# Kernel optimization log

Measured on AMD Instinct MI355X. Metric: run time of the kernel, lower is better.

The kernel has to match this reference:

```python
import jax, jax.numpy as jnp
import numpy as np

HIDDEN = 1024
N_HEADS = 16
HEAD = HIDDEN // N_HEADS  # 64
DFF = 4 * HIDDEN


def setup_inputs() -> dict:
    key = jax.random.key(0)
    ks = jax.random.split(key, 12)
    B, T = 4, 2048
    s = 0.02
    return {
        "x": jax.random.normal(ks[0], (B, T, HIDDEN), jnp.float32),
        # per-head QKV weights, stacked: [H, HIDDEN, HEAD] (no bias, as in Head)
        "Wq": jax.random.normal(ks[1], (N_HEADS, HIDDEN, HEAD), jnp.float32) * s,
        "Wk": jax.random.normal(ks[2], (N_HEADS, HIDDEN, HEAD), jnp.float32) * s,
        "Wv": jax.random.normal(ks[3], (N_HEADS, HIDDEN, HEAD), jnp.float32) * s,
        "Wo": jax.random.normal(ks[4], (HIDDEN, HIDDEN), jnp.float32) * s,
        "bo": jnp.zeros((HIDDEN,), jnp.float32),
        "W1": jax.random.normal(ks[5], (HIDDEN, DFF), jnp.float32) * s,
        "b1": jnp.zeros((DFF,), jnp.float32),
        "W2": jax.random.normal(ks[6], (DFF, HIDDEN), jnp.float32) * s,
        "b2": jnp.zeros((HIDDEN,), jnp.float32),
        "g1": jnp.ones((HIDDEN,), jnp.float32),
        "be1": jnp.zeros((HIDDEN,), jnp.float32),
        "g2": jnp.ones((HIDDEN,), jnp.float32),
        "be2": jnp.zeros((HIDDEN,), jnp.float32),
    }


def _layernorm(x, g, b, eps=1e-5):
    mu = jnp.mean(x, axis=-1, keepdims=True)
    var = jnp.mean(jnp.square(x - mu), axis=-1, keepdims=True)
    return (x - mu) * jax.lax.rsqrt(var + eps) * g + b


def _attention(h, Wq, Wk, Wv, Wo, bo):
    B, T, C = h.shape
    # [B,T,C] x [H,C,D] -> [B,H,T,D]
    Q = jnp.einsum('btc,hcd->bhtd', h, Wq)
    K = jnp.einsum('btc,hcd->bhtd', h, Wk)
    V = jnp.einsum('btc,hcd->bhtd', h, Wv)
    scores = jnp.einsum('bhtd,bhsd->bhts', Q, K) / np.sqrt(HEAD).astype(np.float32)
    causal = jnp.tril(jnp.ones((T, T), bool))
    scores = jnp.where(causal, scores, -jnp.inf)
    attn = jax.nn.softmax(scores, axis=-1)
    out = jnp.einsum('bhts,bhsd->bhtd', attn, V)
    # concat heads in order (head axis -> last dim blocks)
    out = out.transpose(0, 2, 1, 3).reshape(B, T, C)
    return out @ Wo + bo


def reference(x, Wq, Wk, Wv, Wo, bo, W1, b1, W2, b2, g1, be1, g2, be2):
    x = x + _attention(_layernorm(x, g1, be1), Wq, Wk, Wv, Wo, bo)
    h = _layernorm(x, g2, be2)
    ff = jax.nn.relu(h @ W1 + b1) @ W2 + b2
    return x + ff
```

## Files before the change

### kernel.cpp

```cpp
#include <hip/hip_runtime.h>
#include <hip/hip_bf16.h>
#include <stdint.h>


#define HID 1024
#define NH 16
#define HD 64
#define DFF 4096
#define BATCH 4
#define SEQ 2048
#define NTOK (BATCH*SEQ)

typedef unsigned short u16;
typedef unsigned int u32;
typedef __attribute__((ext_vector_type(4))) float f32x4;
typedef __attribute__((ext_vector_type(16))) float f32x16;
typedef __attribute__((ext_vector_type(8))) __bf16 bf16x8;

__device__ __forceinline__ u16 f2bf(float f) {
    unsigned int u = __float_as_uint(f);
    u = (u + 0x7fffu + ((u >> 16) & 1u)) >> 16;
    return (u16)u;
}

__device__ __forceinline__ u32 cvtpk(float lo, float hi) {
    u32 d;
    asm("v_cvt_pk_bf16_f32 %0, %1, %2" : "=v"(d) : "v"(lo), "v"(hi));
    return d;
}

__device__ __forceinline__ void plswap(u32& a, u32& b) {
    asm volatile("v_permlane32_swap_b32 %0, %1" : "+v"(a), "+v"(b));
}

__device__ __forceinline__ void gload_lds16(const void* g, void* lds) {
    __builtin_amdgcn_global_load_lds(
        (const __attribute__((address_space(1))) unsigned int*)(uintptr_t)g,
        (__attribute__((address_space(3))) unsigned int*)(uintptr_t)lds, 16, 0, 0);
}

__global__ __launch_bounds__(256) void ln_kernel(const float* __restrict__ x,
                                                 const float* __restrict__ g,
                                                 const float* __restrict__ be,
                                                 u16* __restrict__ out) {
    __shared__ float red[10];
    const int row = blockIdx.x, tid = threadIdx.x;
    const float4 v = ((const float4*)(x + (size_t)row * HID))[tid];
    float s  = v.x + v.y + v.z + v.w;
    float s2 = v.x*v.x + v.y*v.y + v.z*v.z + v.w*v.w;
    for (int off = 32; off > 0; off >>= 1) {
        s  += __shfl_down(s, off, 64);
        s2 += __shfl_down(s2, off, 64);
    }
    if ((tid & 63) == 0) { red[tid >> 6] = s; red[4 + (tid >> 6)] = s2; }
    __syncthreads();
    if (tid == 0) {
        red[8] = red[0] + red[1] + red[2] + red[3];
        red[9] = red[4] + red[5] + red[6] + red[7];
    }
    __syncthreads();
    const float mu  = red[8] * (1.f / HID);
    const float var = red[9] * (1.f / HID) - mu * mu;
    const float rstd = rsqrtf(var + 1e-5f);
    const float4 g4 = ((const float4*)g)[tid];
    const float4 b4 = ((const float4*)be)[tid];
    ushort4 o;
    o.x = f2bf((v.x - mu) * rstd * g4.x + b4.x);
    o.y = f2bf((v.y - mu) * rstd * g4.y + b4.y);
    o.z = f2bf((v.z - mu) * rstd * g4.z + b4.z);
    o.w = f2bf((v.w - mu) * rstd * g4.w + b4.w);
    ((ushort4*)(out + (size_t)row * HID))[tid] = o;
}

__global__ __launch_bounds__(256) void transpose_w(const float* __restrict__ in,
                                                   u16* __restrict__ out, int R, int C) {
    __shared__ float t[32][33];
    const int r0 = blockIdx.x * 32, c0 = blockIdx.y * 32;
    const float* inb = in + (size_t)blockIdx.z * R * C;
    u16* outb = out + (size_t)blockIdx.z * R * C;
    const int tid = threadIdx.x;
    const int tr = tid >> 3, tc = (tid & 7) * 4;
    const float4 v = *(const float4*)&inb[(size_t)(r0 + tr) * C + c0 + tc];
    t[tr][tc] = v.x; t[tr][tc + 1] = v.y; t[tr][tc + 2] = v.z; t[tr][tc + 3] = v.w;
    __syncthreads();
    ushort4 o;
    o.x = f2bf(t[tc + 0][tr]);
    o.y = f2bf(t[tc + 1][tr]);
    o.z = f2bf(t[tc + 2][tr]);
    o.w = f2bf(t[tc + 3][tr]);
    *(ushort4*)&outb[(size_t)(c0 + tr) * R + r0 + tc] = o;
}

__global__ __launch_bounds__(256) void transpose_v(const u16* __restrict__ in,
                                                   u16* __restrict__ out) {
    __shared__ u16 t[64][65];
    const int s0 = blockIdx.x * 64;
    const size_t bh = blockIdx.y;
    const u16* inb = in + bh * SEQ * HD;
    u16* outb = out + bh * HD * SEQ;
    const int tid = threadIdx.x;
    const int r = tid >> 2, c = (tid & 3) * 16;
    bf16x8 a = *(const bf16x8*)&inb[(size_t)(s0 + r) * HD + c];
    bf16x8 b = *(const bf16x8*)&inb[(size_t)(s0 + r) * HD + c + 8];
    #pragma unroll
    for (int i = 0; i < 8; i++) {
        t[r][c + i]     = ((const u16*)&a)[i];
        t[r][c + 8 + i] = ((const u16*)&b)[i];
    }
    __syncthreads();
    u16 o0[8], o1[8];
    #pragma unroll
    for (int i = 0; i < 8; i++) { o0[i] = t[c + i][r]; o1[i] = t[c + 8 + i][r]; }
    *(bf16x8*)&outb[(size_t)r * SEQ + s0 + c]     = *(const bf16x8*)o0;
    *(bf16x8*)&outb[(size_t)r * SEQ + s0 + c + 8] = *(const bf16x8*)o1;
}

template <int MODE>
__global__ __launch_bounds__(256) void gemm_kernel(const u16* __restrict__ A,
                                                   const u16* __restrict__ B,
                                                   float* __restrict__ outf,
                                                   u16* __restrict__ outh,
                                                   const float* __restrict__ bias,
                                                   const float* __restrict__ resid,
                                                   int K, int N) {
    __shared__ u16 Al[128][32];
    __shared__ u16 Bl[128][32];
    const int tid = threadIdx.x;
    const int w = tid >> 6, l = tid & 63;
    const int wr = w >> 1, wc = w & 1;
    const int m0 = blockIdx.x * 128, n0 = blockIdx.y * 128;

    f32x4 acc[4][4] = {};

    const u16* Ag = A + (size_t)(m0 + w * 32) * K;
    const u16* Bg = B + (size_t)(n0 + w * 32) * K;
    const int lr = l >> 2;
    const int lc = (l & 3) * 8;

    for (int k0 = 0; k0 < K; k0 += 32) {
        __syncthreads();
        #pragma unroll
        for (int it = 0; it < 2; it++) {
            gload_lds16(Ag + (size_t)(it * 16 + lr) * K + k0 + lc, &Al[w * 32 + it * 16][0]);
            gload_lds16(Bg + (size_t)(it * 16 + lr) * K + k0 + lc, &Bl[w * 32 + it * 16][0]);
        }
        __syncthreads();
        bf16x8 af[4], bfr[4];
        #pragma unroll
        for (int i = 0; i < 4; i++)
            af[i] = *(const bf16x8*)&Al[wr * 64 + i * 16 + (l & 15)][(l >> 4) * 8];
        #pragma unroll
        for (int i = 0; i < 4; i++)
            bfr[i] = *(const bf16x8*)&Bl[wc * 64 + i * 16 + (l & 15)][(l >> 4) * 8];
        #pragma unroll
        for (int mi = 0; mi < 4; mi++)
            #pragma unroll
            for (int nj = 0; nj < 4; nj++)
                acc[mi][nj] = __builtin_amdgcn_mfma_f32_16x16x32_bf16(af[mi], bfr[nj], acc[mi][nj], 0, 0, 0);
    }

    const int r00 = m0 + wr * 64 + ((l >> 4) << 2);
    const int c00 = n0 + wc * 64 + (l & 15);
    if (MODE == 0) {
        #pragma unroll
        for (int nj = 0; nj < 4; nj++) {
            const int c = c00 + nj * 16;
            const int which = c >> 10, hc = c & 1023;
            const int h = hc >> 6, d = hc & 63;
            const float sc2 = (which == 0) ? 0.125f : 1.0f;
            u16* outp = outh + (size_t)which * ((size_t)NTOK * HID);
            #pragma unroll
            for (int mi = 0; mi < 4; mi++)
                #pragma unroll
                for (int j = 0; j < 4; j++) {
                    const int r = r00 + mi * 16 + j;
                    const int b = r >> 11, t = r & (SEQ - 1);
                    outp[((size_t)(b * NH + h) * SEQ + t) * HD + d] = f2bf(acc[mi][nj][j] * sc2);
                }
        }
    } else if (MODE == 1) {
        #pragma unroll
        for (int nj = 0; nj < 4; nj++) {
            const int c = c00 + nj * 16;
            const float bi = bias[c];
            #pragma unroll
            for (int mi = 0; mi < 4; mi++)
                #pragma unroll
                for (int j = 0; j < 4; j++) {
                    const int r = r00 + mi * 16 + j;
                    const size_t idx = (size_t)r * N + c;
                    outf[idx] = resid[idx] + acc[mi][nj][j] + bi;
                }
        }
    } else {
        #pragma unroll
        for (int nj = 0; nj < 4; nj++) {
            const int c = c00 + nj * 16;
            const float bi = bias[c];
            #pragma unroll
            for (int mi = 0; mi < 4; mi++)
                #pragma unroll
                for (int j = 0; j < 4; j++) {
                    const int r = r00 + mi * 16 + j;
                    const float v = acc[mi][nj][j] + bi;
                    outh[(size_t)r * N + c] = f2bf(v > 0.f ? v : 0.f);
                }
        }
    }
}

__global__ __launch_bounds__(256) void attn_kernel(const u16* __restrict__ Q,
                                                   const u16* __restrict__ K,
                                                   const u16* __restrict__ Vt,
                                                   u16* __restrict__ O) {
    __shared__ u16 Kl[2][64 * 64];
    __shared__ u16 Vl[2][64 * 64];
    const int qt = (gridDim.x - 1) - blockIdx.x;
    const int bh = blockIdx.y;
    const int tid = threadIdx.x, w = tid >> 6, l = tid & 63;
    const int q32 = l & 31, hi = l >> 5;
    const int qbase = qt * 128 + w * 32;
    const int qrow = qbase + q32;

    const u16* Qg = Q + ((size_t)bh * SEQ + qrow) * HD;
    bf16x8 qf[4];
    #pragma unroll
    for (int c = 0; c < 4; ++c)
        qf[c] = *(const bf16x8*)&Qg[c * 16 + hi * 8];

    f32x16 oa[2] = {};
    float m = -1e30f, lsum = 0.f;

    const u16* Kg0 = K + (size_t)bh * SEQ * HD;
    const u16* Vg0 = Vt + (size_t)bh * HD * SEQ;
    const int sr = tid >> 2;
    const int scb = (tid & 3) * 32;

    bf16x8 kreg[2], vreg[2];
    auto load_tile = [&](int st) {
        const char* Kg = (const char*)(Kg0 + (size_t)st * 64 * HD);
        const char* Vg = (const char*)(Vg0 + st * 64);
        #pragma unroll
        for (int it = 0; it < 2; it++) {
            kreg[it] = *(const bf16x8*)(Kg + (size_t)sr * 128 + scb + it * 16);
            vreg[it] = *(const bf16x8*)(Vg + (size_t)sr * (SEQ * 2) + scb + it * 16);
        }
    };
    auto write_tile = [&](int buf) {
        char* KlB = (char*)Kl[buf];
        char* VlB = (char*)Vl[buf];
        const int sw = (sr & 7) << 4;
        #pragma unroll
        for (int it = 0; it < 2; it++) {
            *(bf16x8*)(KlB + sr * 128 + ((scb + it * 16) ^ sw)) = kreg[it];
            *(bf16x8*)(VlB + sr * 128 + ((scb + it * 16) ^ sw)) = vreg[it];
        }
    };

    const int ntiles = 2 * qt + 2;
    const int tlast = (qbase + 31) >> 6;

    load_tile(0);
    write_tile(0);

    for (int st = 0; st < ntiles; ++st) {
        const int cur = st & 1;
        __syncthreads();
        const bool pf = (st + 1 < ntiles);
        if (pf) load_tile(st + 1);

        if (st <= tlast) {
            const char* KlB = (const char*)Kl[cur];
            const char* VlB = (const char*)Vl[cur];

            f32x16 s[2];
            __builtin_amdgcn_s_setprio(1);
            #pragma unroll
            for (int a = 0; a < 2; ++a) {
                const int row = a * 32 + q32;
                const char* base = KlB + row * 128;
                const int sw = (row & 7) << 4;
                f32x16 accs = {};
                #pragma unroll
                for (int ds4 = 0; ds4 < 4; ++ds4) {
                    bf16x8 kf = *(const bf16x8*)(base + ((ds4 * 32 + hi * 16) ^ sw));
                    accs = __builtin_amdgcn_mfma_f32_32x32x16_bf16(kf, qf[ds4], accs, 0, 0, 0);
                }
                s[a] = accs;
            }
            __builtin_amdgcn_s_setprio(0);

            if (st == tlast) {
                const int st64 = st * 64;
                #pragma unroll
                for (int a = 0; a < 2; ++a)
                    #pragma unroll
                    for (int r = 0; r < 16; ++r) {
                        const int kvg = st64 + a * 32 + (r & 3) + 8 * (r >> 2) + 4 * hi;
                        if (kvg > qrow) s[a][r] = -1e30f;
                    }
            }

            float pm0 = -1e30f, pm1 = -1e30f, pm2 = -1e30f, pm3 = -1e30f;
            #pragma unroll
            for (int r = 0; r < 16; r += 4) {
                pm0 = fmaxf(pm0, fmaxf(s[0][r + 0], s[1][r + 0]));
                pm1 = fmaxf(pm1, fmaxf(s[0][r + 1], s[1][r + 1]));
                pm2 = fmaxf(pm2, fmaxf(s[0][r + 2], s[1][r + 2]));
                pm3 = fmaxf(pm3, fmaxf(s[0][r + 3], s[1][r + 3]));
            }
            float pmax = fmaxf(fmaxf(pm0, pm1), fmaxf(pm2, pm3));
            pmax = fmaxf(pmax, __shfl_xor(pmax, 32, 64));

            if (!__all(pmax <= m + 8.f)) {
                const float newm = fmaxf(m, pmax);
                const float sc = __expf(m - newm);
                m = newm;
                lsum *= sc;
                #pragma unroll
                for (int d = 0; d < 2; ++d)
                    #pragma unroll
                    for (int r = 0; r < 16; ++r)
                        oa[d][r] *= sc;
            }

            float s0 = 0.f, s1 = 0.f, s2 = 0.f, s3 = 0.f;
            #pragma unroll
            for (int a = 0; a < 2; ++a)
                #pragma unroll
                for (int r = 0; r < 16; r += 4) {
                    float p0 = __expf(s[a][r + 0] - m);
                    float p1 = __expf(s[a][r + 1] - m);
                    float p2 = __expf(s[a][r + 2] - m);
                    float p3 = __expf(s[a][r + 3] - m);
                    s[a][r + 0] = p0; s[a][r + 1] = p1;
                    s[a][r + 2] = p2; s[a][r + 3] = p3;
                    s0 += p0; s1 += p1; s2 += p2; s3 += p3;
                }
            float psum = (s0 + s1) + (s2 + s3);
            psum += __shfl_xor(psum, 32, 64);
            lsum += psum;

            u32 W[2][4][2];
            #pragma unroll
            for (int a = 0; a < 2; ++a)
                #pragma unroll
                for (int i = 0; i < 4; ++i) {
                    W[a][i][0] = cvtpk(s[a][4 * i + 0], s[a][4 * i + 1]);
                    W[a][i][1] = cvtpk(s[a][4 * i + 2], s[a][4 * i + 3]);
                }
            bf16x8 pa[4];
            #pragma unroll
            for (int a = 0; a < 2; ++a)
                #pragma unroll
                for (int j = 0; j < 2; ++j) {
                    u32 a0 = W[a][2 * j][0], b0 = W[a][2 * j + 1][0];
                    u32 a1 = W[a][2 * j][1], b1 = W[a][2 * j + 1][1];
                    plswap(a0, b0);
                    plswap(a1, b1);
                    union { u32 ww[4]; bf16x8 v; } u_;
                    u_.ww[0] = a0; u_.ww[1] = a1; u_.ww[2] = b0; u_.ww[3] = b1;
                    pa[2 * a + j] = u_.v;
                }

            __builtin_amdgcn_s_setprio(1);
            #pragma unroll
            for (int dblk = 0; dblk < 2; ++dblk) {
                const int row = dblk * 32 + q32;
                const char* base = VlB + row * 128;
                const int sw = (row & 7) << 4;
                #pragma unroll
                for (int s4 = 0; s4 < 4; ++s4) {
                    bf16x8 vf = *(const bf16x8*)(base + ((s4 * 32 + hi * 16) ^ sw));
                    oa[dblk] = __builtin_amdgcn_mfma_f32_32x32x16_bf16(vf, pa[s4], oa[dblk], 0, 0, 0);
                }
            }
            __builtin_amdgcn_s_setprio(0);
        }

        if (pf) write_tile(cur ^ 1);
    }

    const int b = bh >> 4, h = bh & 15;
    const float inv = 1.f / lsum;
    u16* Orow = O + ((size_t)b * SEQ + qrow) * HID + h * HD;
    #pragma unroll
    for (int dblk = 0; dblk < 2; ++dblk)
        #pragma unroll
        for (int i = 0; i < 4; ++i) {
            ushort4 st4;
            st4.x = f2bf(oa[dblk][4 * i + 0] * inv);
            st4.y = f2bf(oa[dblk][4 * i + 1] * inv);
            st4.z = f2bf(oa[dblk][4 * i + 2] * inv);
            st4.w = f2bf(oa[dblk][4 * i + 3] * inv);
            *(ushort4*)&Orow[dblk * 32 + 8 * i + 4 * hi] = st4;
        }
}

extern "C" void kernel_launch(void* const* d_in, const int* in_sizes, int n_in,
                              void* d_out, int out_size, void* d_ws, size_t ws_size,
                              hipStream_t stream) {
    (void)in_sizes; (void)n_in; (void)out_size; (void)ws_size;
    const float* x   = (const float*)d_in[0];
    const float* Wq  = (const float*)d_in[1];
    const float* Wk  = (const float*)d_in[2];
    const float* Wv  = (const float*)d_in[3];
    const float* Wo  = (const float*)d_in[4];
    const float* bo  = (const float*)d_in[5];
    const float* W1  = (const float*)d_in[6];
    const float* b1  = (const float*)d_in[7];
    const float* W2  = (const float*)d_in[8];
    const float* b2  = (const float*)d_in[9];
    const float* g1  = (const float*)d_in[10];
    const float* be1 = (const float*)d_in[11];
    const float* g2  = (const float*)d_in[12];
    const float* be2 = (const float*)d_in[13];
    float* out = (float*)d_out;

    char* ws = (char*)d_ws;
    size_t off = 0;
    auto alloc = [&](size_t bytes) { void* p = ws + off; off += bytes; return p; };
    u16* Wqkv_t = (u16*)alloc((size_t)3 * HID * HID * 2);
    u16* Wo_t = (u16*)alloc((size_t)HID * HID * 2);
    u16* W1_t = (u16*)alloc((size_t)DFF * HID * 2);
    u16* W2_t = (u16*)alloc((size_t)HID * DFF * 2);
    u16* h1   = (u16*)alloc((size_t)NTOK * HID * 2);
    u16* Qb   = (u16*)alloc((size_t)NTOK * HID * 2);
    u16* Kb   = (u16*)alloc((size_t)NTOK * HID * 2);
    u16* Vb   = (u16*)alloc((size_t)NTOK * HID * 2);
    u16* Vt   = (u16*)alloc((size_t)NTOK * HID * 2);
    float* x2 = (float*)alloc((size_t)NTOK * HID * 4);
    u16* ff1  = Qb;

    transpose_w<<<dim3(32, 2, 16), 256, 0, stream>>>(Wq, Wqkv_t, HID, HD);
    transpose_w<<<dim3(32, 2, 16), 256, 0, stream>>>(Wk, Wqkv_t + (size_t)HID * HID, HID, HD);
    transpose_w<<<dim3(32, 2, 16), 256, 0, stream>>>(Wv, Wqkv_t + (size_t)2 * HID * HID, HID, HD);
    transpose_w<<<dim3(32, 32, 1), 256, 0, stream>>>(Wo, Wo_t, HID, HID);
    transpose_w<<<dim3(32, 128, 1), 256, 0, stream>>>(W1, W1_t, HID, DFF);
    transpose_w<<<dim3(128, 32, 1), 256, 0, stream>>>(W2, W2_t, DFF, HID);

    ln_kernel<<<NTOK, 256, 0, stream>>>(x, g1, be1, h1);

    gemm_kernel<0><<<dim3(64, 24), 256, 0, stream>>>(h1, Wqkv_t, nullptr, Qb,
                                                     nullptr, nullptr, HID, 3072);

    transpose_v<<<dim3(SEQ / 64, BATCH * NH), 256, 0, stream>>>(Vb, Vt);

    u16* attn_out = Vb;
    attn_kernel<<<dim3(SEQ / 128, BATCH * NH), 256, 0, stream>>>(Qb, Kb, Vt, attn_out);

    gemm_kernel<1><<<dim3(64, 8), 256, 0, stream>>>(attn_out, Wo_t, x2, nullptr, bo, x, HID, HID);

    ln_kernel<<<NTOK, 256, 0, stream>>>(x2, g2, be2, h1);

    gemm_kernel<2><<<dim3(64, 32), 256, 0, stream>>>(h1, W1_t, nullptr, ff1, b1, nullptr, HID, DFF);

    gemm_kernel<1><<<dim3(64, 8), 256, 0, stream>>>(ff1, W2_t, out, nullptr, b2, x2, DFF, HID);
}
```

Before: 583.7 us.

## Replace GEMM with 4-stage async LDS pipeline and larger swizzled tiles

```diff
diff --git a/kernel.cpp b/kernel.cpp
--- a/kernel.cpp
+++ b/kernel.cpp
@@ -37,6 +37,21 @@
     __builtin_amdgcn_global_load_lds(
         (const __attribute__((address_space(1))) unsigned int*)(uintptr_t)g,
         (__attribute__((address_space(3))) unsigned int*)(uintptr_t)lds, 16, 0, 0);
+}
+
+template <int N>
+__device__ __forceinline__ void waitvm() {
+    if constexpr (N == 8)      asm volatile("s_waitcnt vmcnt(8)" ::: "memory");
+    else if constexpr (N == 6) asm volatile("s_waitcnt vmcnt(6)" ::: "memory");
+    else if constexpr (N == 4) asm volatile("s_waitcnt vmcnt(4)" ::: "memory");
+    else if constexpr (N == 3) asm volatile("s_waitcnt vmcnt(3)" ::: "memory");
+    else                       asm volatile("s_waitcnt vmcnt(0)" ::: "memory");
+}
+
+__device__ __forceinline__ void pipe_barrier() {
+    __builtin_amdgcn_sched_barrier(0);
+    __builtin_amdgcn_s_barrier();
+    __builtin_amdgcn_sched_barrier(0);
 }
 
 __global__ __launch_bounds__(256) void ln_kernel(const float* __restrict__ x,
@@ -115,92 +130,150 @@
     *(bf16x8*)&outb[(size_t)r * SEQ + s0 + c + 8] = *(const bf16x8*)o1;
 }
 
-template <int MODE>
-__global__ __launch_bounds__(256) void gemm_kernel(const u16* __restrict__ A,
-                                                   const u16* __restrict__ B,
-                                                   float* __restrict__ outf,
-                                                   u16* __restrict__ outh,
-                                                   const float* __restrict__ bias,
-                                                   const float* __restrict__ resid,
-                                                   int K, int N) {
-    __shared__ u16 Al[128][32];
-    __shared__ u16 Bl[128][32];
+template <int BN, int MODE>
+__global__ __launch_bounds__(512, 2) void gemm_p(const u16* __restrict__ A,
+                                                 const u16* __restrict__ B,
+                                                 float* __restrict__ outf,
+                                                 u16* __restrict__ outh,
+                                                 const float* __restrict__ bias,
+                                                 const float* __restrict__ resid,
+                                                 int K, int N) {
+    constexpr int ASL = 16384;
+    constexpr int BSL = (BN == 256) ? 16384 : 8192;
+    constexpr int BRD = (BN == 256) ? 2 : 1;
+    constexpr int LPS = 2 + BRD;
+    constexpr int WN  = (BN == 256) ? 4 : 2;
+    constexpr int MR  = (BN == 256) ? 128 : 64;
+    constexpr int MF  = MR / 16;
+    __shared__ char lds[4 * ASL + 4 * BSL];
+    char* const ldsB = lds + 4 * ASL;
+
     const int tid = threadIdx.x;
     const int w = tid >> 6, l = tid & 63;
-    const int wr = w >> 1, wc = w & 1;
-    const int m0 = blockIdx.x * 128, n0 = blockIdx.y * 128;
-
-    f32x4 acc[4][4] = {};
-
-    const u16* Ag = A + (size_t)(m0 + w * 32) * K;
-    const u16* Bg = B + (size_t)(n0 + w * 32) * K;
-    const int lr = l >> 2;
-    const int lc = (l & 3) * 8;
-
-    for (int k0 = 0; k0 < K; k0 += 32) {
-        __syncthreads();
-        #pragma unroll
-        for (int it = 0; it < 2; it++) {
-            gload_lds16(Ag + (size_t)(it * 16 + lr) * K + k0 + lc, &Al[w * 32 + it * 16][0]);
-            gload_lds16(Bg + (size_t)(it * 16 + lr) * K + k0 + lc, &Bl[w * 32 + it * 16][0]);
-        }
-        __syncthreads();
-        bf16x8 af[4], bfr[4];
-        #pragma unroll
-        for (int i = 0; i < 4; i++)
-            af[i] = *(const bf16x8*)&Al[wr * 64 + i * 16 + (l & 15)][(l >> 4) * 8];
-        #pragma unroll
-        for (int i = 0; i < 4; i++)
-            bfr[i] = *(const bf16x8*)&Bl[wc * 64 + i * 16 + (l & 15)][(l >> 4) * 8];
-        #pragma unroll
-        for (int mi = 0; mi < 4; mi++)
-            #pragma unroll
-            for (int nj = 0; nj < 4; nj++)
-                acc[mi][nj] = __builtin_amdgcn_mfma_f32_16x16x32_bf16(af[mi], bfr[nj], acc[mi][nj], 0, 0, 0);
-    }
-
-    const int r00 = m0 + wr * 64 + ((l >> 4) << 2);
-    const int c00 = n0 + wc * 64 + (l & 15);
-    if (MODE == 0) {
-        #pragma unroll
-        for (int nj = 0; nj < 4; nj++) {
-            const int c = c00 + nj * 16;
+    const int l15 = l & 15, lg = l >> 4;
+    const int wr = w / WN, wc = w % WN;
+    const int m0 = (blockIdx.x & 31) * 256;
+    const int n0 = (blockIdx.x >> 5) * BN;
+    const size_t Kb = (size_t)K * 2;
+    const int H = K >> 5;
+
+    int gar[2], gac[2], gbr[BRD], gbc[BRD];
+    #pragma unroll
+    for (int rd = 0; rd < 2; ++rd) {
+        const int p = rd * 8192 + tid * 16;
+        const int line = p >> 7, s16 = (p >> 4) & 7;
+        const int u = (s16 * 16) ^ ((line & 7) << 4);
+        gar[rd] = line + ((u >> 6) & 1) * 128;
+        gac[rd] = u & 63;
+    }
+    #pragma unroll
+    for (int rd = 0; rd < BRD; ++rd) {
+        const int p = rd * 8192 + tid * 16;
+        const int line = p >> 7, s16 = (p >> 4) & 7;
+        const int u = (s16 * 16) ^ ((line & 7) << 4);
+        gbr[rd] = line + ((u >> 6) & 1) * ((BN == 256) ? 128 : 64);
+        gbc[rd] = u & 63;
+    }
+
+    const char* Ag = (const char*)A + (size_t)m0 * Kb;
+    const char* Bg = (const char*)B + (size_t)n0 * Kb;
+
+    auto stage = [&](int h) {
+        const int slot = h & 3;
+        const size_t kby = (size_t)h * 64;
+        #pragma unroll
+        for (int rd = 0; rd < 2; ++rd)
+            gload_lds16(Ag + (size_t)gar[rd] * Kb + kby + gac[rd],
+                        lds + slot * ASL + rd * 8192 + w * 1024);
+        #pragma unroll
+        for (int rd = 0; rd < BRD; ++rd)
+            gload_lds16(Bg + (size_t)gbr[rd] * Kb + kby + gbc[rd],
+                        ldsB + slot * BSL + rd * 8192 + w * 1024);
+    };
+
+    int offA[MF], offB[4];
+    #pragma unroll
+    for (int mi = 0; mi < MF; ++mi) {
+        const int row = wr * MR + mi * 16 + l15;
+        offA[mi] = (row & 127) * 128 + ((((row >> 7) * 64) + lg * 16) ^ ((l15 & 7) << 4));
+    }
+    #pragma unroll
+    for (int nj = 0; nj < 4; ++nj) {
+        const int row = wc * 64 + nj * 16 + l15;
+        if (BN == 256)
+            offB[nj] = (row & 127) * 128 + ((((row >> 7) * 64) + lg * 16) ^ ((l15 & 7) << 4));
+        else
+            offB[nj] = (row & 63) * 128 + ((((row >> 6) * 64) + lg * 16) ^ ((l15 & 7) << 4));
+    }
+
+    f32x4 acc[MF][4] = {};
+
+    auto compute = [&](int hh) {
+        const char* la = lds + (hh & 3) * ASL;
+        const char* lb = ldsB + (hh & 3) * BSL;
+        bf16x8 af[MF], bf[4];
+        #pragma unroll
+        for (int mi = 0; mi < MF; ++mi) af[mi] = *(const bf16x8*)(la + offA[mi]);
+        #pragma unroll
+        for (int nj = 0; nj < 4; ++nj) bf[nj] = *(const bf16x8*)(lb + offB[nj]);
+        __builtin_amdgcn_s_setprio(1);
+        #pragma unroll
+        for (int mi = 0; mi < MF; ++mi)
+            #pragma unroll
+            for (int nj = 0; nj < 4; ++nj)
+                acc[mi][nj] = __builtin_amdgcn_mfma_f32_16x16x32_bf16(af[mi], bf[nj], acc[mi][nj], 0, 0, 0);
+        __builtin_amdgcn_s_setprio(0);
+    };
+
+    stage(0); stage(1); stage(2);
+    waitvm<2 * LPS>();
+    pipe_barrier();
+
+    int h = 0;
+    for (; h < H - 3; ++h) {
+        compute(h);
+        stage(h + 3);
+        waitvm<2 * LPS>();
+        pipe_barrier();
+    }
+    compute(h); waitvm<LPS>(); pipe_barrier(); ++h;
+    compute(h); waitvm<0>();   pipe_barrier(); ++h;
+    compute(h);
+
+    const int r00 = m0 + wr * MR + (lg << 2);
+    const int c00 = n0 + wc * 64 + l15;
+    #pragma unroll
+    for (int nj = 0; nj < 4; ++nj) {
+        const int c = c00 + nj * 16;
+        if (MODE == 0) {
             const int which = c >> 10, hc = c & 1023;
-            const int h = hc >> 6, d = hc & 63;
+            const int hh = hc >> 6, d = hc & 63;
             const float sc2 = (which == 0) ? 0.125f : 1.0f;
             u16* outp = outh + (size_t)which * ((size_t)NTOK * HID);
             #pragma unroll
-            for (int mi = 0; mi < 4; mi++)
-                #pragma unroll
-                for (int j = 0; j < 4; j++) {
+            for (int mi = 0; mi < MF; ++mi)
+                #pragma unroll
+                for (int j = 0; j < 4; ++j) {
                     const int r = r00 + mi * 16 + j;
                     const int b = r >> 11, t = r & (SEQ - 1);
-                    outp[((size_t)(b * NH + h) * SEQ + t) * HD + d] = f2bf(acc[mi][nj][j] * sc2);
-                }
-        }
-    } else if (MODE == 1) {
-        #pragma unroll
-        for (int nj = 0; nj < 4; nj++) {
-            const int c = c00 + nj * 16;
+                    outp[((size_t)(b * NH + hh) * SEQ + t) * HD + d] = f2bf(acc[mi][nj][j] * sc2);
+                }
+        } else if (MODE == 1) {
             const float bi = bias[c];
             #pragma unroll
-            for (int mi = 0; mi < 4; mi++)
-                #pragma unroll
-                for (int j = 0; j < 4; j++) {
+            for (int mi = 0; mi < MF; ++mi)
+                #pragma unroll
+                for (int j = 0; j < 4; ++j) {
                     const int r = r00 + mi * 16 + j;
                     const size_t idx = (size_t)r * N + c;
                     outf[idx] = resid[idx] + acc[mi][nj][j] + bi;
                 }
-        }
-    } else {
-        #pragma unroll
-        for (int nj = 0; nj < 4; nj++) {
-            const int c = c00 + nj * 16;
+        } else {
             const float bi = bias[c];
             #pragma unroll
-            for (int mi = 0; mi < 4; mi++)
-                #pragma unroll
-                for (int j = 0; j < 4; j++) {
+            for (int mi = 0; mi < MF; ++mi)
+                #pragma unroll
+                for (int j = 0; j < 4; ++j) {
                     const int r = r00 + mi * 16 + j;
                     const float v = acc[mi][nj][j] + bi;
                     outh[(size_t)r * N + c] = f2bf(v > 0.f ? v : 0.f);
@@ -233,8 +306,8 @@
 
     const u16* Kg0 = K + (size_t)bh * SEQ * HD;
     const u16* Vg0 = Vt + (size_t)bh * HD * SEQ;
-    const int sr = tid >> 2;
-    const int scb = (tid & 3) * 32;
+    const int sr8 = tid >> 3;
+    const int sc8 = (tid & 7) * 16;
 
     bf16x8 kreg[2], vreg[2];
     auto load_tile = [&](int st) {
@@ -242,18 +315,18 @@
         const char* Vg = (const char*)(Vg0 + st * 64);
         #pragma unroll
         for (int it = 0; it < 2; it++) {
-            kreg[it] = *(const bf16x8*)(Kg + (size_t)sr * 128 + scb + it * 16);
-            vreg[it] = *(const bf16x8*)(Vg + (size_t)sr * (SEQ * 2) + scb + it * 16);
+            kreg[it] = *(const bf16x8*)(Kg + (size_t)(it * 32 + sr8) * 128 + sc8);
+            vreg[it] = *(const bf16x8*)(Vg + (size_t)(it * 32 + sr8) * (SEQ * 2) + sc8);
         }
     };
     auto write_tile = [&](int buf) {
         char* KlB = (char*)Kl[buf];
         char* VlB = (char*)Vl[buf];
-        const int sw = (sr & 7) << 4;
+        const int sw = (sr8 & 7) << 4;
         #pragma unroll
         for (int it = 0; it < 2; it++) {
-            *(bf16x8*)(KlB + sr * 128 + ((scb + it * 16) ^ sw)) = kreg[it];
-            *(bf16x8*)(VlB + sr * 128 + ((scb + it * 16) ^ sw)) = vreg[it];
+            *(bf16x8*)(KlB + (it * 32 + sr8) * 128 + (sc8 ^ sw)) = kreg[it];
+            *(bf16x8*)(VlB + (it * 32 + sr8) * 128 + (sc8 ^ sw)) = vreg[it];
         }
     };
 
@@ -441,19 +514,19 @@
 
     ln_kernel<<<NTOK, 256, 0, stream>>>(x, g1, be1, h1);
 
-    gemm_kernel<0><<<dim3(64, 24), 256, 0, stream>>>(h1, Wqkv_t, nullptr, Qb,
-                                                     nullptr, nullptr, HID, 3072);
+    gemm_p<128, 0><<<dim3(32 * 24), 512, 0, stream>>>(h1, Wqkv_t, nullptr, Qb,
+                                                      nullptr, nullptr, HID, 3072);
 
     transpose_v<<<dim3(SEQ / 64, BATCH * NH), 256, 0, stream>>>(Vb, Vt);
 
     u16* attn_out = Vb;
     attn_kernel<<<dim3(SEQ / 128, BATCH * NH), 256, 0, stream>>>(Qb, Kb, Vt, attn_out);
 
-    gemm_kernel<1><<<dim3(64, 8), 256, 0, stream>>>(attn_out, Wo_t, x2, nullptr, bo, x, HID, HID);
+    gemm_p<128, 1><<<dim3(32 * 8), 512, 0, stream>>>(attn_out, Wo_t, x2, nullptr, bo, x, HID, HID);
 
     ln_kernel<<<NTOK, 256, 0, stream>>>(x2, g2, be2, h1);
 
-    gemm_kernel<2><<<dim3(64, 32), 256, 0, stream>>>(h1, W1_t, nullptr, ff1, b1, nullptr, HID, DFF);
-
-    gemm_kernel<1><<<dim3(64, 8), 256, 0, stream>>>(ff1, W2_t, out, nullptr, b2, x2, DFF, HID);
-}
+    gemm_p<256, 2><<<dim3(32 * 16), 512, 0, stream>>>(h1, W1_t, nullptr, ff1, b1, nullptr, HID, DFF);
+
+    gemm_p<128, 1><<<dim3(32 * 8), 512, 0, stream>>>(ff1, W2_t, out, nullptr, b2, x2, DFF, HID);
+}
```

Result: faster. 561.2 us (-3.9%).
